# Optimization experiments

Measured on AMD Instinct MI355X. Metric: run time of the kernel, lower is better.

The kernel has to match this reference:

```python
import jax, jax.numpy as jnp
import numpy as np

B, N, C, H = 8, 1568, 384, 6
D = C // H
SCALE = D ** -0.5
EPS = 1e-6


def setup_inputs() -> dict:
    key = jax.random.key(0)
    k1, k2, k3, k4 = jax.random.split(key, 4)
    x = jax.random.normal(k1, (B, N, C), dtype=jnp.float32)
    # binary token-keep policy (0/1), as produced by the pruning module
    vis_tube = jax.random.randint(k2, (B, N, 1), 0, 2).astype(jnp.float32)
    w_qkv = jax.random.normal(k3, (3 * C, C), dtype=jnp.float32) * (C ** -0.5)
    w_proj = jax.random.normal(k4, (C, C), dtype=jnp.float32) * (C ** -0.5)
    b_proj = jnp.zeros((C,), dtype=jnp.float32)
    return {"x": x, "vis_tube": vis_tube, "w_qkv": w_qkv, "w_proj": w_proj, "b_proj": b_proj}


def _attn_forward(x, vis_tube, w_qkv, w_proj, b_proj):
    qkv = (x @ w_qkv.T).reshape(B, N, 3, H, D)
    qkv = jnp.transpose(qkv, (2, 0, 3, 1, 4))  # [3,B,H,N,D]
    q, k, v = qkv[0], qkv[1], qkv[2]

    attn = jnp.einsum('bhnd,bhmd->bhnm', q, k) * SCALE  # [B,H,N,N]

    # softmax_with_policy: mask keys by policy, but always keep the diagonal
    policy = vis_tube.reshape(B, 1, 1, N)
    eye = jnp.eye(N, dtype=policy.dtype).reshape(1, 1, N, N)
    attn_policy = policy + (1.0 - policy) * eye  # [B,1,N,N]

    max_att = jnp.max(attn, axis=-1, keepdims=True)
    e = jnp.exp(attn - max_att) * attn_policy
    attn = (e + EPS / N) / (jnp.sum(e, axis=-1, keepdims=True) + EPS)

    out = jnp.einsum('bhnm,bhmd->bhnd', attn, v)  # [B,H,N,D]
    out = jnp.transpose(out, (0, 2, 1, 3)).reshape(B, N, C)
    return out @ w_proj.T + b_proj


def reference(x, vis_tube, w_qkv, w_proj, b_proj):
    return _attn_forward(x, vis_tube, w_qkv, w_proj, b_proj)
```

## Files before the change

### kernel.cpp

```cpp
#include <hip/hip_runtime.h>

#define B_ 8
#define N_ 1568
#define NPAD_ 1600
#define C_ 384
#define H_ 6
#define D_ 64
#define BH_ 48
#define SZ_ (B_*H_*N_*D_)
#define EPS_ 1e-6f
#define CSC_ 0.18033688011112042f

typedef short s16x8 __attribute__((ext_vector_type(8)));
typedef short s16x4 __attribute__((ext_vector_type(4)));
typedef float f32x4 __attribute__((ext_vector_type(4)));

static __device__ __forceinline__ ushort f2bf(float f){
  union { float f; unsigned u; } v; v.f = f;
  unsigned r = v.u + 0x7fffu + ((v.u >> 16) & 1u);
  return (ushort)(r >> 16);
}
static __device__ __forceinline__ unsigned cvtpk(float lo, float hi){
  unsigned r;
  asm("v_cvt_pk_bf16_f32 %0, %1, %2" : "=v"(r) : "v"(lo), "v"(hi));
  return r;
}
#define MFMA16(a,b,c) __builtin_amdgcn_mfma_f32_16x16x32_bf16((a),(b),(c),0,0,0)

#if __has_builtin(__builtin_amdgcn_exp2f)
#define EXP2F(x) __builtin_amdgcn_exp2f(x)
#else
#define EXP2F(x) exp2f(x)
#endif

#define POLPAD_ (B_*NPAD_)
__global__ __launch_bounds__(256) void pol_pad_k(const float* __restrict__ vis, float* __restrict__ pp){
  int i = blockIdx.x*256 + threadIdx.x;
  if (i < POLPAD_){
    int b = i / NPAD_, n = i - b*NPAD_;
    pp[i] = (n < N_) ? vis[b*N_ + n] : 0.f;
  }
}

#define XV8_ 602112
#define WQ8_ 55296
#define WP8_ 18432
__global__ __launch_bounds__(256) void cvt_all(const float* __restrict__ X, const float* __restrict__ Wq,
                                               const float* __restrict__ Wp, ushort* __restrict__ Xb,
                                               ushort* __restrict__ Wqb, ushort* __restrict__ Wpb){
  int i = blockIdx.x*256 + threadIdx.x;
  const float* src; ushort* dst; int off;
  if (i < XV8_)            { src = X;  dst = Xb;  off = i; }
  else if (i < XV8_+WQ8_)  { src = Wq; dst = Wqb; off = i - XV8_; }
  else                     { src = Wp; dst = Wpb; off = i - XV8_ - WQ8_; }
  float4 a = ((const float4*)src)[off*2];
  float4 b = ((const float4*)src)[off*2+1];
  s16x8 r;
  r[0]=(short)f2bf(a.x); r[1]=(short)f2bf(a.y); r[2]=(short)f2bf(a.z); r[3]=(short)f2bf(a.w);
  r[4]=(short)f2bf(b.x); r[5]=(short)f2bf(b.y); r[6]=(short)f2bf(b.z); r[7]=(short)f2bf(b.w);
  *(s16x8*)&dst[off*8] = r;
}

__global__ __launch_bounds__(256) void qkv_gemm(const ushort* __restrict__ Xb, const ushort* __restrict__ Wb,
                                                ushort* __restrict__ Qg, ushort* __restrict__ Kg,
                                                ushort* __restrict__ Vg, ushort* __restrict__ Vtg,
                                                int vmode){
  __shared__ __align__(16) ushort Al[128*40];
  __shared__ __align__(16) ushort Bl[128*40];
  const int tid = threadIdx.x, lane = tid&63, w = tid>>6;
  const int g = lane>>4, lr = lane&15;
  const int wr = w>>1, wc = w&1;
  const int m0 = blockIdx.x*128, j0 = blockIdx.y*128;
  const int ar = tid>>1, ah = tid&1;
  f32x4 acc[4][4];
  #pragma unroll
  for (int i=0;i<4;i++)
    #pragma unroll
    for (int j=0;j<4;j++) acc[i][j]=(f32x4){0,0,0,0};

  for (int ks=0; ks<384; ks+=32){
    const ushort* as = Xb + (size_t)(m0+ar)*384 + ks + ah*16;
    s16x8 a0 = ((const s16x8*)as)[0];
    s16x8 a1 = ((const s16x8*)as)[1];
    const ushort* bs = Wb + (size_t)(j0+ar)*384 + ks + ah*16;
    s16x8 b0 = ((const s16x8*)bs)[0];
    s16x8 b1 = ((const s16x8*)bs)[1];
    *(s16x8*)&Al[ar*40 + ah*16]     = a0;
    *(s16x8*)&Al[ar*40 + ah*16 + 8] = a1;
    *(s16x8*)&Bl[ar*40 + ah*16]     = b0;
    *(s16x8*)&Bl[ar*40 + ah*16 + 8] = b1;
    __syncthreads();
    s16x8 af[4], bf[4];
    #pragma unroll
    for (int fm=0; fm<4; fm++) af[fm] = *(const s16x8*)&Al[(wr*64+fm*16+lr)*40 + g*8];
    #pragma unroll
    for (int fn=0; fn<4; fn++) bf[fn] = *(const s16x8*)&Bl[(wc*64+fn*16+lr)*40 + g*8];
    #pragma unroll
    for (int fm=0; fm<4; fm++)
      #pragma unroll
      for (int fn=0; fn<4; fn++)
        acc[fm][fn] = MFMA16(af[fm], bf[fn], acc[fm][fn]);
    __syncthreads();
  }
  #pragma unroll
  for (int fm=0; fm<4; fm++){
    #pragma unroll
    for (int jj=0; jj<4; jj++){
      int m = m0 + wr*64 + fm*16 + g*4 + jj;
      int bi = m / N_; int n = m - bi*N_;
      #pragma unroll
      for (int fn=0; fn<4; fn++){
        int j = j0 + wc*64 + fn*16 + lr;
        int t = j/384, jc = j - t*384;
        int h = jc>>6, d = jc&63;
        float v = acc[fm][fn][jj];
        if (t==0)      Qg[((size_t)(bi*H_+h)*N_ + n)*64 + d] = f2bf(v * CSC_);
        else if (t==1) Kg[((size_t)(bi*H_+h)*N_ + n)*64 + d] = f2bf(v);
        else {
          if (vmode) Vg[((size_t)(bi*H_+h)*N_ + n)*64 + d] = f2bf(v);
          else       Vtg[((size_t)(bi*H_+h)*64 + d)*N_ + n] = f2bf(v);
        }
      }
    }
  }
}

__global__ __launch_bounds__(256) void v_tr(const ushort* __restrict__ Vg, ushort* __restrict__ Vt){
  __shared__ ushort lds[32*72];
  const int bh = blockIdx.x, k0 = blockIdx.y*32;
  const int tid = threadIdx.x;
  const int r = tid>>3, dc = (tid&7)*8;
  *(s16x8*)&lds[r*72 + dc] = *(const s16x8*)&Vg[((size_t)bh*N_ + k0 + r)*64 + dc];
  __syncthreads();
  const int d = tid>>2, kc = (tid&3)*8;
  s16x8 o;
  #pragma unroll
  for (int i=0;i<8;i++) o[i] = (short)lds[(kc+i)*72 + d];
  *(s16x8*)&Vt[((size_t)bh*64 + d)*N_ + k0 + kc] = o;
}

#define LOADK(D0,D1,TT) do{ \
  _Pragma("unroll") \
  for (int kg=0;kg<4;kg++){ \
    int kr = (TT)+kg*16+lr; kr = kr<N_?kr:N_-1; \
    const ushort* kp = Kbh + (size_t)kr*64; \
    D0[kg] = *(const s16x8*)(kp + g*8); \
    D1[kg] = *(const s16x8*)(kp + 32 + g*8); } }while(0)

#define LOADV(TT) do{ \
  _Pragma("unroll") \
  for (int fd=0;fd<4;fd++){ \
    const ushort* vp = Vbh + (size_t)(fd*16+lr)*N_ + (TT); \
    va0_[fd] = *(const s16x8*)(vp + g*8); \
    va1_[fd] = *(const s16x8*)(vp + 32 + g*8); } }while(0)

#define LOADP(TT) do{ \
  _Pragma("unroll") \
  for (int kg=0;kg<4;kg++) pmv[kg] = *(const float4*)&polp[(TT) + kg*16 + 4*g]; }while(0)

#define PROC(KC0,KC1,QF0,QF1,OO,MM,LL,QQ,DG,T0) do{ \
  f32x4 st[4]; \
  __builtin_amdgcn_s_setprio(1); \
  _Pragma("unroll") \
  for (int kg=0;kg<4;kg++){ f32x4 z=(f32x4){0,0,0,0}; z=MFMA16(KC0[kg],QF0,z); st[kg]=MFMA16(KC1[kg],QF1,z); } \
  __builtin_amdgcn_s_setprio(0); \
  float pmax; { \
    float x0=fmaxf(fmaxf(st[0][0],st[0][1]),fmaxf(st[0][2],st[0][3])); \
    float x1=fmaxf(fmaxf(st[1][0],st[1][1]),fmaxf(st[1][2],st[1][3])); \
    float x2=fmaxf(fmaxf(st[2][0],st[2][1]),fmaxf(st[2][2],st[2][3])); \
    float x3=fmaxf(fmaxf(st[3][0],st[3][1]),fmaxf(st[3][2],st[3][3])); \
    pmax=fmaxf(fmaxf(x0,x1),fmaxf(x2,x3)); \
    pmax=fmaxf(pmax,__shfl_xor(pmax,16)); pmax=fmaxf(pmax,__shfl_xor(pmax,32)); } \
  if (__any(pmax > (MM)+8.f)){ \
    float Mn=fmaxf((MM),pmax); float corr=EXP2F((MM)-Mn); (LL)*=corr; \
    _Pragma("unroll") for (int fd=0;fd<4;fd++){ OO[fd][0]*=corr;OO[fd][1]*=corr;OO[fd][2]*=corr;OO[fd][3]*=corr; } \
    (MM)=Mn; } \
  _Pragma("unroll") \
  for (int kg=0;kg<4;kg++){ \
    _Pragma("unroll") \
    for (int jj=0;jj<4;jj++){ \
      float e=EXP2F(st[kg][jj]-(MM)); float em=e*((&pmv[kg].x)[jj]); \
      int key=(T0)+kg*16+4*g+jj; \
      st[kg][jj]=((DG)&&key==(QQ))?e:em; } } \
  { float se=(st[0][0]+st[0][1])+(st[0][2]+st[0][3]); \
    se+=(st[1][0]+st[1][1])+(st[1][2]+st[1][3]); \
    se+=(st[2][0]+st[2][1])+(st[2][2]+st[2][3]); \
    se+=(st[3][0]+st[3][1])+(st[3][2]+st[3][3]); \
    se+=__shfl_xor(se,16); se+=__shfl_xor(se,32); (LL)+=se; } \
  unsigned pk[4][2]; \
  _Pragma("unroll") \
  for (int kg=0;kg<4;kg++){ pk[kg][0]=cvtpk(st[kg][0],st[kg][1]); pk[kg][1]=cvtpk(st[kg][2],st[kg][3]); } \
  union { unsigned u[4]; s16x8 v; } bfr[2]; \
  _Pragma("unroll") \
  for (int kh=0;kh<2;kh++){ \
    _Pragma("unroll") \
    for (int wd=0;wd<4;wd++){ \
      int srcl=(wd<2)?sl0:sl1; \
      unsigned q0_=(unsigned)__shfl((int)pk[2*kh][wd&1],srcl); \
      unsigned q1_=(unsigned)__shfl((int)pk[2*kh+1][wd&1],srcl); \
      bfr[kh].u[wd]=(g<2)?q0_:q1_; } } \
  __builtin_amdgcn_s_setprio(1); \
  _Pragma("unroll") \
  for (int fd=0;fd<4;fd++){ OO[fd]=MFMA16(va0_[fd],bfr[0].v,OO[fd]); OO[fd]=MFMA16(va1_[fd],bfr[1].v,OO[fd]); } \
  __builtin_amdgcn_s_setprio(0); \
}while(0)

__global__ __launch_bounds__(64,2) void attn_fwd(const ushort* __restrict__ Qg, const ushort* __restrict__ Kg,
                                                 const ushort* __restrict__ Vt, const float* __restrict__ pol,
                                                 ushort* __restrict__ AO){
  const int lane = threadIdx.x & 63;
  const int g = lane>>4, lr = lane&15;
  const int bh = blockIdx.x; const int b = bh / H_, h = bh - b*H_;
  const int qbase = blockIdx.y*32;
  const int qA = qbase + lr, qB = qbase + 16 + lr;
  const ushort* QrA = Qg + ((size_t)bh*N_ + qA)*64;
  const ushort* QrB = Qg + ((size_t)bh*N_ + qB)*64;
  const s16x8 qa0 = *(const s16x8*)(QrA + g*8);
  const s16x8 qa1 = *(const s16x8*)(QrA + 32 + g*8);
  const s16x8 qb0 = *(const s16x8*)(QrB + g*8);
  const s16x8 qb1 = *(const s16x8*)(QrB + 32 + g*8);
  const float* polp = pol + b*NPAD_;
  const ushort* Kbh = Kg + (size_t)bh*N_*64;
  const ushort* Vbh = Vt + (size_t)bh*64*N_;
  const int sl0 = ((lane>>4)&1)<<5 | lr;
  const int sl1 = sl0 + 16;
  const int dbase = qbase & ~63;

  f32x4 oA[4], oB[4];
  #pragma unroll
  for (int i=0;i<4;i++){ oA[i]=(f32x4){0,0,0,0}; oB[i]=(f32x4){0,0,0,0}; }
  float MA=-INFINITY, LA=0.f, MB=-INFINITY, LB=0.f;

  s16x8 ka0[4], ka1[4], kb0[4], kb1[4], va0_[4], va1_[4];
  float4 pmv[4];

  LOADK(ka0, ka1, 0);
  #pragma unroll 1
  for (int it=0; it<12; it++){
    const int t0 = it*128;
    LOADV(t0); LOADP(t0);
    LOADK(kb0, kb1, t0+64);
    __builtin_amdgcn_sched_barrier(0);
    PROC(ka0,ka1, qa0,qa1, oA,MA,LA,qA, (dbase==t0), t0);
    PROC(ka0,ka1, qb0,qb1, oB,MB,LB,qB, (dbase==t0), t0);
    const int t1 = t0+64;
    LOADV(t1); LOADP(t1);
    LOADK(ka0, ka1, t1+64);
    __builtin_amdgcn_sched_barrier(0);
    PROC(kb0,kb1, qa0,qa1, oA,MA,LA,qA, (dbase==t1), t1);
    PROC(kb0,kb1, qb0,qb1, oB,MB,LB,qB, (dbase==t1), t1);
  }
  {
    const int t0 = 1536;
    LOADV(t0); LOADP(t0);
    PROC(ka0,ka1, qa0,qa1, oA,MA,LA,qA, (dbase==t0), t0);
    PROC(ka0,ka1, qb0,qb1, oB,MB,LB,qB, (dbase==t0), t0);
  }

  {
    float inv = 1.f / (LA + EPS_);
    ushort* aop = AO + ((size_t)b*N_ + qA)*C_ + h*64 + 4*g;
    #pragma unroll
    for (int fd=0; fd<4; fd++){
      s16x4 r;
      r[0]=(short)f2bf(oA[fd][0]*inv); r[1]=(short)f2bf(oA[fd][1]*inv);
      r[2]=(short)f2bf(oA[fd][2]*inv); r[3]=(short)f2bf(oA[fd][3]*inv);
      *(s16x4*)(aop + fd*16) = r;
    }
  }
  {
    float inv = 1.f / (LB + EPS_);
    ushort* aop = AO + ((size_t)b*N_ + qB)*C_ + h*64 + 4*g;
    #pragma unroll
    for (int fd=0; fd<4; fd++){
      s16x4 r;
      r[0]=(short)f2bf(oB[fd][0]*inv); r[1]=(short)f2bf(oB[fd][1]*inv);
      r[2]=(short)f2bf(oB[fd][2]*inv); r[3]=(short)f2bf(oB[fd][3]*inv);
      *(s16x4*)(aop + fd*16) = r;
    }
  }
}

__global__ __launch_bounds__(256) void proj_gemm(const ushort* __restrict__ A, const ushort* __restrict__ Wb,
                                                 const float* __restrict__ bias, float* __restrict__ out){
  __shared__ __align__(16) ushort Al[128*40];
  __shared__ __align__(16) ushort Bl[128*40];
  const int tid = threadIdx.x, lane = tid&63, w = tid>>6;
  const int g = lane>>4, lr = lane&15;
  const int wr = w>>1, wc = w&1;
  const int m0 = blockIdx.x*128, j0 = blockIdx.y*128;
  const int ar = tid>>1, ah = tid&1;
  f32x4 acc[4][4];
  #pragma unroll
  for (int i=0;i<4;i++)
    #pragma unroll
    for (int j=0;j<4;j++) acc[i][j]=(f32x4){0,0,0,0};

  for (int ks=0; ks<384; ks+=32){
    const ushort* as = A + (size_t)(m0+ar)*384 + ks + ah*16;
    s16x8 a0 = ((const s16x8*)as)[0];
    s16x8 a1 = ((const s16x8*)as)[1];
    const ushort* bs = Wb + (size_t)(j0+ar)*384 + ks + ah*16;
    s16x8 b0 = ((const s16x8*)bs)[0];
    s16x8 b1 = ((const s16x8*)bs)[1];
    *(s16x8*)&Al[ar*40 + ah*16]     = a0;
    *(s16x8*)&Al[ar*40 + ah*16 + 8] = a1;
    *(s16x8*)&Bl[ar*40 + ah*16]     = b0;
    *(s16x8*)&Bl[ar*40 + ah*16 + 8] = b1;
    __syncthreads();
    s16x8 af[4], bf[4];
    #pragma unroll
    for (int fm=0; fm<4; fm++) af[fm] = *(const s16x8*)&Al[(wr*64+fm*16+lr)*40 + g*8];
    #pragma unroll
    for (int fn=0; fn<4; fn++) bf[fn] = *(const s16x8*)&Bl[(wc*64+fn*16+lr)*40 + g*8];
    #pragma unroll
    for (int fm=0; fm<4; fm++)
      #pragma unroll
      for (int fn=0; fn<4; fn++)
        acc[fm][fn] = MFMA16(af[fm], bf[fn], acc[fm][fn]);
    __syncthreads();
  }
  float bsv[4];
  #pragma unroll
  for (int fn=0; fn<4; fn++) bsv[fn] = bias[j0 + wc*64 + fn*16 + lr];
  #pragma unroll
  for (int fm=0; fm<4; fm++){
    #pragma unroll
    for (int jj=0; jj<4; jj++){
      int m = m0 + wr*64 + fm*16 + g*4 + jj;
      #pragma unroll
      for (int fn=0; fn<4; fn++){
        int j = j0 + wc*64 + fn*16 + lr;
        out[(size_t)m*384 + j] = acc[fm][fn][jj] + bsv[fn];
      }
    }
  }
}

extern "C" void kernel_launch(void* const* d_in, const int* in_sizes, int n_in,
                              void* d_out, int out_size, void* d_ws, size_t ws_size,
                              hipStream_t stream) {
  const float* x     = (const float*)d_in[0];
  const float* vis   = (const float*)d_in[1];
  const float* wqkv  = (const float*)d_in[2];
  const float* wproj = (const float*)d_in[3];
  const float* bproj = (const float*)d_in[4];
  float* out = (float*)d_out;

  ushort* Qg  = (ushort*)d_ws;
  ushort* Kg  = Qg + SZ_;
  ushort* Vtg = Kg + SZ_;
  ushort* AO  = Vtg + SZ_;
  ushort* Xb  = AO;
  ushort* Vg  = AO + SZ_;
  size_t need_tr = (size_t)5*SZ_*2 + (size_t)(3*C_*C_ + C_*C_)*2 + (size_t)POLPAD_*4;
  int tr = (ws_size >= need_tr) ? 1 : 0;
  ushort* Wqb = tr ? (Vg + SZ_) : (Vg);
  ushort* Wpb = Wqb + 3*C_*C_;
  float*  pol_pad = (float*)(Wpb + C_*C_);

  pol_pad_k<<<(POLPAD_+255)/256, 256, 0, stream>>>(vis, pol_pad);
  cvt_all<<<2640, 256, 0, stream>>>(x, wqkv, wproj, Xb, Wqb, Wpb);
  qkv_gemm<<<dim3(98,9), 256, 0, stream>>>(Xb, Wqb, Qg, Kg, Vg, Vtg, tr);
  if (tr) v_tr<<<dim3(48,49), 256, 0, stream>>>(Vg, Vtg);
  attn_fwd<<<dim3(48,49), 64, 0, stream>>>(Qg, Kg, Vtg, pol_pad, AO);
  proj_gemm<<<dim3(98,3), 256, 0, stream>>>(AO, Wpb, bproj, out);
}
```

Baseline: 252.2 us.

## Share K/V tiles across four waves via double-buffered LDS in attention

The attention kernel changes from one wave per 32 queries, each loading K and V straight from global memory into registers, to a 256-thread block of four waves covering 128 queries. The block cooperatively stages each 64-key K/V tile into double-buffered shared memory, so global K/V traffic drops by up to four times. The block index is remapped for XCD locality and the last query block is guarded. The policy-padding kernel is also merged into the conversion kernel, removing one launch. In exchange, each tile now needs a __syncthreads and LDS reads, and the last query block is partly idle.

```diff
diff --git a/kernel.cpp b/kernel.cpp
--- a/kernel.cpp
+++ b/kernel.cpp
@@ -33,32 +33,34 @@
 #define EXP2F(x) exp2f(x)
 #endif
 
-#define POLPAD_ (B_*NPAD_)
-__global__ __launch_bounds__(256) void pol_pad_k(const float* __restrict__ vis, float* __restrict__ pp){
-  int i = blockIdx.x*256 + threadIdx.x;
-  if (i < POLPAD_){
-    int b = i / NPAD_, n = i - b*NPAD_;
-    pp[i] = (n < N_) ? vis[b*N_ + n] : 0.f;
-  }
-}
-
 #define XV8_ 602112
 #define WQ8_ 55296
 #define WP8_ 18432
-__global__ __launch_bounds__(256) void cvt_all(const float* __restrict__ X, const float* __restrict__ Wq,
-                                               const float* __restrict__ Wp, ushort* __restrict__ Xb,
-                                               ushort* __restrict__ Wqb, ushort* __restrict__ Wpb){
+#define TOT8_ (XV8_+WQ8_+WP8_)
+#define POLPAD_ (B_*NPAD_)
+__global__ __launch_bounds__(256) void cvt_pol(const float* __restrict__ X, const float* __restrict__ Wq,
+                                               const float* __restrict__ Wp, const float* __restrict__ vis,
+                                               ushort* __restrict__ Xb, ushort* __restrict__ Wqb,
+                                               ushort* __restrict__ Wpb, float* __restrict__ pp){
   int i = blockIdx.x*256 + threadIdx.x;
-  const float* src; ushort* dst; int off;
-  if (i < XV8_)            { src = X;  dst = Xb;  off = i; }
-  else if (i < XV8_+WQ8_)  { src = Wq; dst = Wqb; off = i - XV8_; }
-  else                     { src = Wp; dst = Wpb; off = i - XV8_ - WQ8_; }
-  float4 a = ((const float4*)src)[off*2];
-  float4 b = ((const float4*)src)[off*2+1];
-  s16x8 r;
-  r[0]=(short)f2bf(a.x); r[1]=(short)f2bf(a.y); r[2]=(short)f2bf(a.z); r[3]=(short)f2bf(a.w);
-  r[4]=(short)f2bf(b.x); r[5]=(short)f2bf(b.y); r[6]=(short)f2bf(b.z); r[7]=(short)f2bf(b.w);
-  *(s16x8*)&dst[off*8] = r;
+  if (i < TOT8_){
+    const float* src; ushort* dst; int off;
+    if (i < XV8_)            { src = X;  dst = Xb;  off = i; }
+    else if (i < XV8_+WQ8_)  { src = Wq; dst = Wqb; off = i - XV8_; }
+    else                     { src = Wp; dst = Wpb; off = i - XV8_ - WQ8_; }
+    float4 a = ((const float4*)src)[off*2];
+    float4 b = ((const float4*)src)[off*2+1];
+    s16x8 r;
+    r[0]=(short)f2bf(a.x); r[1]=(short)f2bf(a.y); r[2]=(short)f2bf(a.z); r[3]=(short)f2bf(a.w);
+    r[4]=(short)f2bf(b.x); r[5]=(short)f2bf(b.y); r[6]=(short)f2bf(b.z); r[7]=(short)f2bf(b.w);
+    *(s16x8*)&dst[off*8] = r;
+  } else {
+    int p = i - TOT8_;
+    if (p < POLPAD_){
+      int b = p / NPAD_, n = p - b*NPAD_;
+      pp[p] = (n < N_) ? vis[b*N_ + n] : 0.f;
+    }
+  }
 }
 
 __global__ __launch_bounds__(256) void qkv_gemm(const ushort* __restrict__ Xb, const ushort* __restrict__ Wb,
@@ -139,30 +141,35 @@
   *(s16x8*)&Vt[((size_t)bh*64 + d)*N_ + k0 + kc] = o;
 }
 
-#define LOADK(D0,D1,TT) do{ \
-  _Pragma("unroll") \
-  for (int kg=0;kg<4;kg++){ \
-    int kr = (TT)+kg*16+lr; kr = kr<N_?kr:N_-1; \
-    const ushort* kp = Kbh + (size_t)kr*64; \
-    D0[kg] = *(const s16x8*)(kp + g*8); \
-    D1[kg] = *(const s16x8*)(kp + 32 + g*8); } }while(0)
-
-#define LOADV(TT) do{ \
-  _Pragma("unroll") \
-  for (int fd=0;fd<4;fd++){ \
-    const ushort* vp = Vbh + (size_t)(fd*16+lr)*N_ + (TT); \
-    va0_[fd] = *(const s16x8*)(vp + g*8); \
-    va1_[fd] = *(const s16x8*)(vp + 32 + g*8); } }while(0)
+#define LDST_ 72
 
 #define LOADP(TT) do{ \
   _Pragma("unroll") \
   for (int kg=0;kg<4;kg++) pmv[kg] = *(const float4*)&polp[(TT) + kg*16 + 4*g]; }while(0)
 
-#define PROC(KC0,KC1,QF0,QF1,OO,MM,LL,QQ,DG,T0) do{ \
+#define STAGEISSUE(T0N) do{ \
+  int kr_ = (T0N)+sr; kr_ = kr_<N_?kr_:N_-1; \
+  const ushort* kp_ = Kbh + (size_t)kr_*64 + sc2*8; \
+  sk0 = *(const s16x8*)(kp_); sk1 = *(const s16x8*)(kp_+8); \
+  const ushort* vp_ = Vbh + (size_t)sr*N_ + (T0N) + sc2*8; \
+  sv0 = *(const s16x8*)(vp_); sv1 = *(const s16x8*)(vp_+8); \
+}while(0)
+
+#define STAGEWRITE(KD,VD) do{ \
+  *(s16x8*)&(KD)[sr*LDST_ + sc2*8]     = sk0; \
+  *(s16x8*)&(KD)[sr*LDST_ + sc2*8 + 8] = sk1; \
+  *(s16x8*)&(VD)[sr*LDST_ + sc2*8]     = sv0; \
+  *(s16x8*)&(VD)[sr*LDST_ + sc2*8 + 8] = sv1; }while(0)
+
+#define PROCQ(KB,VB,QF0,QF1,OO,MM,LL,QQ,DG,T0) do{ \
   f32x4 st[4]; \
   __builtin_amdgcn_s_setprio(1); \
   _Pragma("unroll") \
-  for (int kg=0;kg<4;kg++){ f32x4 z=(f32x4){0,0,0,0}; z=MFMA16(KC0[kg],QF0,z); st[kg]=MFMA16(KC1[kg],QF1,z); } \
+  for (int kg=0;kg<4;kg++){ \
+    const ushort* krp_ = (KB) + (kg*16+lr)*LDST_ + g*8; \
+    s16x8 kf0_ = *(const s16x8*)(krp_); \
+    s16x8 kf1_ = *(const s16x8*)(krp_+32); \
+    f32x4 z=(f32x4){0,0,0,0}; z=MFMA16(kf0_,QF0,z); st[kg]=MFMA16(kf1_,QF1,z); } \
   __builtin_amdgcn_s_setprio(0); \
   float pmax; { \
     float x0=fmaxf(fmaxf(st[0][0],st[0][1]),fmaxf(st[0][2],st[0][3])); \
@@ -201,20 +208,40 @@
       bfr[kh].u[wd]=(g<2)?q0_:q1_; } } \
   __builtin_amdgcn_s_setprio(1); \
   _Pragma("unroll") \
-  for (int fd=0;fd<4;fd++){ OO[fd]=MFMA16(va0_[fd],bfr[0].v,OO[fd]); OO[fd]=MFMA16(va1_[fd],bfr[1].v,OO[fd]); } \
+  for (int fd=0;fd<4;fd++){ \
+    const ushort* vrp_ = (VB) + (fd*16+lr)*LDST_ + g*8; \
+    s16x8 va0_ = *(const s16x8*)(vrp_); \
+    s16x8 va1_ = *(const s16x8*)(vrp_+32); \
+    OO[fd]=MFMA16(va0_,bfr[0].v,OO[fd]); OO[fd]=MFMA16(va1_,bfr[1].v,OO[fd]); } \
   __builtin_amdgcn_s_setprio(0); \
 }while(0)
 
-__global__ __launch_bounds__(64,2) void attn_fwd(const ushort* __restrict__ Qg, const ushort* __restrict__ Kg,
-                                                 const ushort* __restrict__ Vt, const float* __restrict__ pol,
-                                                 ushort* __restrict__ AO){
-  const int lane = threadIdx.x & 63;
+#define TILE(KB,VB,T0,STG,T0N,KD,VD) do{ \
+  if (STG){ STAGEISSUE(T0N); __builtin_amdgcn_sched_barrier(0); } \
+  LOADP(T0); \
+  const bool dg_ = ((qA0 & ~63) == (T0)); \
+  PROCQ(KB,VB, qa0,qa1, oA,MA,LA,qA, dg_, T0); \
+  PROCQ(KB,VB, qb0,qb1, oB,MB,LB,qB, dg_, T0); \
+  if (STG){ STAGEWRITE(KD,VD); __syncthreads(); } \
+}while(0)
+
+__global__ __launch_bounds__(256,2) void attn_fwd(const ushort* __restrict__ Qg, const ushort* __restrict__ Kg,
+                                                  const ushort* __restrict__ Vt, const float* __restrict__ pol,
+                                                  ushort* __restrict__ AO){
+  __shared__ __align__(16) ushort Kl0[64*LDST_], Kl1[64*LDST_];
+  __shared__ __align__(16) ushort Vl0[64*LDST_], Vl1[64*LDST_];
+  const int tid = threadIdx.x, lane = tid&63, w = tid>>6;
   const int g = lane>>4, lr = lane&15;
-  const int bh = blockIdx.x; const int b = bh / H_, h = bh - b*H_;
-  const int qbase = blockIdx.y*32;
-  const int qA = qbase + lr, qB = qbase + 16 + lr;
-  const ushort* QrA = Qg + ((size_t)bh*N_ + qA)*64;
-  const ushort* QrB = Qg + ((size_t)bh*N_ + qB)*64;
+  const int orig = blockIdx.x;
+  const int wg = (orig & 7)*78 + (orig >> 3);
+  const int bh = wg / 13, qb = wg - bh*13;
+  const int b = bh / H_, h = bh - b*H_;
+  const int qA0 = qb*128 + w*32;
+  const int qA = qA0 + lr, qB = qA0 + 16 + lr;
+  const int qAc = qA < N_ ? qA : N_-1;
+  const int qBc = qB < N_ ? qB : N_-1;
+  const ushort* QrA = Qg + ((size_t)bh*N_ + qAc)*64;
+  const ushort* QrB = Qg + ((size_t)bh*N_ + qBc)*64;
   const s16x8 qa0 = *(const s16x8*)(QrA + g*8);
   const s16x8 qa1 = *(const s16x8*)(QrA + 32 + g*8);
   const s16x8 qb0 = *(const s16x8*)(QrB + g*8);
@@ -224,40 +251,29 @@
   const ushort* Vbh = Vt + (size_t)bh*64*N_;
   const int sl0 = ((lane>>4)&1)<<5 | lr;
   const int sl1 = sl0 + 16;
-  const int dbase = qbase & ~63;
+  const int sr = tid>>2;
+  const int sc2 = (tid&3)*2;
 
   f32x4 oA[4], oB[4];
   #pragma unroll
   for (int i=0;i<4;i++){ oA[i]=(f32x4){0,0,0,0}; oB[i]=(f32x4){0,0,0,0}; }
   float MA=-INFINITY, LA=0.f, MB=-INFINITY, LB=0.f;
-
-  s16x8 ka0[4], ka1[4], kb0[4], kb1[4], va0_[4], va1_[4];
+  s16x8 sk0, sk1, sv0, sv1;
   float4 pmv[4];
 
-  LOADK(ka0, ka1, 0);
+  STAGEISSUE(0);
+  STAGEWRITE(Kl0, Vl0);
+  __syncthreads();
+
   #pragma unroll 1
-  for (int it=0; it<12; it++){
-    const int t0 = it*128;
-    LOADV(t0); LOADP(t0);
-    LOADK(kb0, kb1, t0+64);
-    __builtin_amdgcn_sched_barrier(0);
-    PROC(ka0,ka1, qa0,qa1, oA,MA,LA,qA, (dbase==t0), t0);
-    PROC(ka0,ka1, qb0,qb1, oB,MB,LB,qB, (dbase==t0), t0);
-    const int t1 = t0+64;
-    LOADV(t1); LOADP(t1);
-    LOADK(ka0, ka1, t1+64);
-    __builtin_amdgcn_sched_barrier(0);
-    PROC(kb0,kb1, qa0,qa1, oA,MA,LA,qA, (dbase==t1), t1);
-    PROC(kb0,kb1, qb0,qb1, oB,MB,LB,qB, (dbase==t1), t1);
-  }
-  {
-    const int t0 = 1536;
-    LOADV(t0); LOADP(t0);
-    PROC(ka0,ka1, qa0,qa1, oA,MA,LA,qA, (dbase==t0), t0);
-    PROC(ka0,ka1, qb0,qb1, oB,MB,LB,qB, (dbase==t0), t0);
-  }
-
-  {
+  for (int p=0; p<12; p++){
+    const int t0 = p*128;
+    TILE(Kl0,Vl0, t0,      1, t0+64,   Kl1,Vl1);
+    TILE(Kl1,Vl1, t0+64,   1, t0+128,  Kl0,Vl0);
+  }
+  TILE(Kl0,Vl0, 1536, 0, 0, Kl0,Vl0);
+
+  if (qA < N_){
     float inv = 1.f / (LA + EPS_);
     ushort* aop = AO + ((size_t)b*N_ + qA)*C_ + h*64 + 4*g;
     #pragma unroll
@@ -268,7 +284,7 @@
       *(s16x4*)(aop + fd*16) = r;
     }
   }
-  {
+  if (qB < N_){
     float inv = 1.f / (LB + EPS_);
     ushort* aop = AO + ((size_t)b*N_ + qB)*C_ + h*64 + 4*g;
     #pragma unroll
@@ -359,10 +375,9 @@
   ushort* Wpb = Wqb + 3*C_*C_;
   float*  pol_pad = (float*)(Wpb + C_*C_);
 
-  pol_pad_k<<<(POLPAD_+255)/256, 256, 0, stream>>>(vis, pol_pad);
-  cvt_all<<<2640, 256, 0, stream>>>(x, wqkv, wproj, Xb, Wqb, Wpb);
+  cvt_pol<<<2690, 256, 0, stream>>>(x, wqkv, wproj, vis, Xb, Wqb, Wpb, pol_pad);
   qkv_gemm<<<dim3(98,9), 256, 0, stream>>>(Xb, Wqb, Qg, Kg, Vg, Vtg, tr);
   if (tr) v_tr<<<dim3(48,49), 256, 0, stream>>>(Vg, Vtg);
-  attn_fwd<<<dim3(48,49), 64, 0, stream>>>(Qg, Kg, Vtg, pol_pad, AO);
+  attn_fwd<<<624, 256, 0, stream>>>(Qg, Kg, Vtg, pol_pad, AO);
   proj_gemm<<<dim3(98,3), 256, 0, stream>>>(AO, Wpb, bproj, out);
 }
```

After: 222.3 us. 1.13x faster.
